# Kernel tuning notes

Measured on AMD Instinct MI355X. Metric: run time of the kernel, lower is better.

Reference implementation:

```python
import jax, jax.numpy as jnp
import numpy as np
from jax import lax

N, D = 65536, 6
NUM_SAMPLES, NUM_GROUPS, EMBED_DIM = 2048, 64, 512
EPS = 1e-5


def farthest_point_sampling(points_xyz, num_samples, key):
    # Sequential FPS via lax.scan: squared-euclidean min-distance update + argmax.
    n = points_xyz.shape[0]
    first = jax.random.randint(key, (), 0, n)
    dists0 = jnp.full((n,), jnp.inf, dtype=points_xyz.dtype)

    def step(carry, _):
        dists, last = carry
        d = jnp.sum((points_xyz - points_xyz[last]) ** 2, axis=-1)  # [n]
        dists = jnp.minimum(dists, d)
        dists = dists.at[last].set(-jnp.inf)  # never re-pick sampled points
        nxt = jnp.argmax(dists)
        return (dists, nxt), nxt

    (_, _), rest = lax.scan(step, (dists0, first), None, length=num_samples - 1)
    return jnp.concatenate([first[None], rest])  # [num_samples]


def bn(x, scale, bias):
    # flax nn.BatchNorm (training stats): normalize over all axes but the last.
    mean = x.mean(axis=(0, 1), keepdims=True)
    var = x.var(axis=(0, 1), keepdims=True)
    return scale * (x - mean) * lax.rsqrt(var + EPS) + bias


def setup_inputs() -> dict:
    key = jax.random.key(0)
    ks = jax.random.split(key, 3)
    points = jax.random.normal(ks[0], (N, D), dtype=jnp.float32)
    W1 = jax.random.normal(ks[1], (2 * D, EMBED_DIM), dtype=jnp.float32) * (1.0 / np.sqrt(2 * D))
    W2 = jax.random.normal(ks[2], (EMBED_DIM, EMBED_DIM), dtype=jnp.float32) * (1.0 / np.sqrt(EMBED_DIM))
    return {
        "points": points,
        "W1": W1, "b1": jnp.zeros((EMBED_DIM,), jnp.float32),
        "scale1": jnp.ones((EMBED_DIM,), jnp.float32), "bias1": jnp.zeros((EMBED_DIM,), jnp.float32),
        "W2": W2, "b2": jnp.zeros((EMBED_DIM,), jnp.float32),
        "scale2": jnp.ones((EMBED_DIM,), jnp.float32), "bias2": jnp.zeros((EMBED_DIM,), jnp.float32),
        "random_key": 1,
    }


def reference(points, W1, b1, scale1, bias1, W2, b2, scale2, bias2, random_key):
    key = jax.random.key(random_key)
    points_xyz = points[:, :3]

    # 1) farthest point sampling -> centroid indices [S]
    sampled_ids = farthest_point_sampling(points_xyz, NUM_SAMPLES, key)
    centroids = points_xyz[sampled_ids]  # [S, 3]

    # 2) KNN via squared-euclidean cdist + approx top-k (matches lax.approx_max_k in source)
    dist = (jnp.sum(centroids ** 2, -1)[:, None]
            + jnp.sum(points_xyz ** 2, -1)[None, :]
            - 2.0 * centroids @ points_xyz.T)  # [S, N]
    groups = lax.approx_max_k(-dist, NUM_GROUPS)[1]  # [S, k] int32

    # 3) gather-group: concat(delta-to-centroid, raw features) -> [S, k, 2D]
    cluster = points[groups]                      # [S, k, D]
    centroid_full = points[sampled_ids]           # [S, D]
    delta = cluster - centroid_full[:, None, :]
    features = jnp.concatenate([delta, cluster], axis=-1)  # [S, k, 2D]

    # 4) Dense + BN + ReLU, twice
    h = jax.nn.relu(bn(features @ W1 + b1, scale1, bias1))  # [S, k, E]
    h = jax.nn.relu(bn(h @ W2 + b2, scale2, bias2))         # [S, k, E]

    # 5) max-pool over the group axis
    return jnp.max(h, axis=1)  # [S, E]
```

## Files before the change

kernel.cpp:

```cpp
#include <hip/hip_runtime.h>
#include <stdint.h>

#define N_PTS 65536
#define DIMS 6
#define NSAMP 2048
#define NGRP 64
#define EMB 512
#define ROWS (NSAMP*NGRP)
#define EPS_BN 1e-5f

#define FIRST_MODE 0

typedef __attribute__((ext_vector_type(8))) short short8;
typedef __attribute__((ext_vector_type(4))) float float4v;

__device__ __forceinline__ unsigned short f2bf(float f) {
  unsigned u = __float_as_uint(f);
  u += 0x7FFFu + ((u >> 16) & 1u);
  return (unsigned short)(u >> 16);
}

__device__ __forceinline__ void tf2x32(unsigned k0, unsigned k1, unsigned &x0, unsigned &x1) {
  unsigned ks[3] = {k0, k1, k0 ^ k1 ^ 0x1BD11BDAu};
  const unsigned R[8] = {13,15,26,6,17,29,16,24};
  x0 += ks[0]; x1 += ks[1];
#pragma unroll
  for (int g = 0; g < 5; ++g) {
#pragma unroll
    for (int j = 0; j < 4; ++j) {
      unsigned r = R[(g & 1) * 4 + j];
      x0 += x1;
      x1 = (x1 << r) | (x1 >> (32 - r));
      x1 ^= x0;
    }
    x0 += ks[(g + 1) % 3];
    x1 += ks[(g + 2) % 3] + (unsigned)(g + 1);
  }
}

__device__ __forceinline__ int compute_first(unsigned seed) {
  unsigned k0 = 0u, k1 = seed;
  unsigned s0, s1;
#if (FIRST_MODE == 0) || (FIRST_MODE == 1)
  { unsigned a0 = 0u, a1 = 1u; tf2x32(k0, k1, a0, a1); s0 = a0; s1 = a1; }
#else
  { unsigned p0 = 0u, p1 = 2u; tf2x32(k0, k1, p0, p1);
    unsigned q0 = 1u, q1 = 3u; tf2x32(k0, k1, q0, q1);
    s0 = p1; s1 = q1; }
#endif
  unsigned b0 = 0u, b1v = 0u; tf2x32(s0, s1, b0, b1v);
#if (FIRST_MODE == 0) || (FIRST_MODE == 3)
  unsigned bits = b0 ^ b1v;
#else
  unsigned bits = b0;
#endif
  return (int)(bits & 0xFFFFu);
}

#define FPSB 16
#define MEGA_BLOCKS 256
#define FPS_PPT 4
#define GB_CAND 512
#define H1B_S 520
#define MEGA_LDS 90112
#define FAST_TRIES 64
#define WARMUP_ITS 4
#define SLOTS ((NSAMP-1)*FPSB)

#define DPPMAX(x, ctrl) do { \
  unsigned _m = (unsigned)__builtin_amdgcn_update_dpp(0, (int)(x), (ctrl), 0xf, 0xf, true); \
  (x) = (x) > _m ? (x) : _m; } while (0)

__device__ __forceinline__ void st_u64_l2(unsigned long long* p, unsigned long long v) {
  asm volatile("global_store_dwordx2 %0, %1, off sc0" :: "v"(p), "v"(v) : "memory");
}
__device__ __forceinline__ unsigned long long ld_u64_l2(const unsigned long long* p) {
  unsigned long long r;
  asm volatile("global_load_dwordx2 %0, %1, off sc0\n\ts_waitcnt vmcnt(0)"
               : "=&v"(r) : "v"(p) : "memory");
  return r;
}

__global__ __launch_bounds__(256) void k_init(const float* __restrict__ pts,
    const float* __restrict__ W2, const int* __restrict__ seed_arr,
    unsigned long long* __restrict__ slot, float* __restrict__ stats,
    float* __restrict__ st2, unsigned short* __restrict__ W2T,
    float4* __restrict__ xyzw, int* __restrict__ sampled) {
  int tid = blockIdx.x * 256 + threadIdx.x;
  if (tid < N_PTS) {
    float x = pts[tid*6], y = pts[tid*6+1], z = pts[tid*6+2];
    float p2 = __fadd_rn(__fadd_rn(__fmul_rn(x,x), __fmul_rn(y,y)), __fmul_rn(z,z));
    xyzw[tid] = make_float4(x, y, z, p2);
  }
#pragma unroll
  for (int i = 0; i < 4; ++i) {
    int e = tid + i*65536;
    int c = e >> 9, k = e & 511;
    W2T[e] = f2bf(W2[k*EMB + c]);
  }
  if (tid < 2*SLOTS) slot[tid] = 0ull;
  if (tid < 4*EMB) stats[tid] = 0.f;
  if (tid < 32*1024) st2[tid] = 0.f;
  if (tid >= 1 && tid < NSAMP) sampled[tid] = -1;
  if (tid == 0) sampled[0] = compute_first((unsigned)seed_arr[0]);
}

__global__ __launch_bounds__(1024) void k_mega(
    const float4* __restrict__ xyzw, const float* __restrict__ pts,
    const float* __restrict__ W1, const float* __restrict__ b1,
    unsigned long long* __restrict__ slot, int* __restrict__ sampled,
    int* __restrict__ groups, float* __restrict__ gsum, float* __restrict__ gss) {
  extern __shared__ __align__(16) char smraw[];
  const int t = threadIdx.x;
  unsigned long long* mirror = slot + SLOTS;
  if ((blockIdx.x & 15) == 0) {
    unsigned long long* blkmax = (unsigned long long*)smraw;
    volatile int* winLDS = (volatile int*)(smraw + 256);
    const int b = blockIdx.x >> 4;
    const int T = b*1024 + t;
    const int lane = t & 63, wid = t >> 6;
    float px[FPS_PPT], py[FPS_PPT], pz[FPS_PPT], pd[FPS_PPT];
    unsigned nidxu[FPS_PPT];
#pragma unroll
    for (int i = 0; i < FPS_PPT; ++i) {
      float4 p = xyzw[T + 16384*i];
      px[i] = p.x; py[i] = p.y; pz[i] = p.z; pd[i] = __builtin_inff();
      nidxu[i] = 0xFFFFFFFFu - (unsigned)(T + 16384*i);
    }
    if (t == 0) { winLDS[0] = -1; winLDS[1] = -1; blkmax[0] = 0ull; blkmax[1] = 0ull; }
    int last = sampled[0] & 0xFFFF;
    bool slowlink = false;
    if (wid == 0) __builtin_amdgcn_s_setprio(3);
    __syncthreads();
    for (int it = 0; it < NSAMP-1; ++it) {
      const int p = it & 1;
      float4 cc = xyzw[last];
      unsigned long long best = 1ull;
#pragma unroll
      for (int i = 0; i < FPS_PPT; ++i) {
        float dx = __fsub_rn(px[i], cc.x);
        float dy = __fsub_rn(py[i], cc.y);
        float dz = __fsub_rn(pz[i], cc.z);
        float d = __fadd_rn(__fadd_rn(__fmul_rn(dx,dx), __fmul_rn(dy,dy)), __fmul_rn(dz,dz));
        pd[i] = fminf(pd[i], d);
        unsigned long long pk = ((unsigned long long)__float_as_uint(pd[i]) << 32)
                              | (unsigned long long)nidxu[i];
        best = best > pk ? best : pk;
      }
      unsigned myd = (unsigned)(best >> 32);
      unsigned r = myd;
      DPPMAX(r, 0x111);
      DPPMAX(r, 0x112);
      DPPMAX(r, 0x114);
      DPPMAX(r, 0x118);
      DPPMAX(r, 0x142);
      DPPMAX(r, 0x143);
      unsigned bd = (unsigned)__builtin_amdgcn_readlane((int)r, 63);
      unsigned long long tie = __ballot(myd == bd);
      unsigned long long wbest;
      if (__popcll(tie) == 1) {
        int wl = (int)__builtin_ctzll(tie);
        unsigned lo = (unsigned)__builtin_amdgcn_readlane((int)(unsigned)best, wl);
        wbest = ((unsigned long long)bd << 32) | (unsigned long long)lo;
      } else {
        wbest = best;
#pragma unroll
        for (int off = 32; off >= 1; off >>= 1) {
          unsigned long long o = __shfl_xor(wbest, off, 64);
          wbest = wbest > o ? wbest : o;
        }
      }
      if (lane == 0) atomicMax(&blkmax[p], wbest);
      __syncthreads();
      if (wid == 0) {
        if (lane == 0) {
          winLDS[1-p] = -1;
          unsigned long long m = blkmax[p];
          blkmax[p] = 0ull;
          st_u64_l2(&mirror[it*FPSB + b], m);
          __hip_atomic_store(&slot[it*FPSB + b], m,
                             __ATOMIC_RELAXED, __HIP_MEMORY_SCOPE_AGENT);
        }
        unsigned long long v = 0ull;
        if (lane < FPSB) {
          unsigned long long* spm = &mirror[it*FPSB + lane];
          unsigned long long* sp  = &slot[it*FPSB + lane];
          if (it >= WARMUP_ITS && !slowlink) {
            int tries = 0;
            do { v = ld_u64_l2(spm); } while (v == 0ull && ++tries < FAST_TRIES);
            if (v == 0ull) slowlink = true;
          }
          if (v == 0ull) {
            do { v = __hip_atomic_load(sp, __ATOMIC_RELAXED, __HIP_MEMORY_SCOPE_AGENT); }
            while (v == 0ull);
          }
        }
        unsigned pd32 = (unsigned)(v >> 32);
        unsigned r2 = pd32;
        DPPMAX(r2, 0x111);
        DPPMAX(r2, 0x112);
        DPPMAX(r2, 0x114);
        DPPMAX(r2, 0x118);
        unsigned bd2 = (unsigned)__builtin_amdgcn_readlane((int)r2, 15);
        unsigned long long tie2 = __ballot((lane < FPSB) && (pd32 == bd2));
        if (__popcll(tie2) == 1) {
          int wl2 = (int)__builtin_ctzll(tie2);
          unsigned lo2 = (unsigned)__builtin_amdgcn_readlane((int)(unsigned)v, wl2);
          v = ((unsigned long long)bd2 << 32) | (unsigned long long)lo2;
        } else {
#pragma unroll
          for (int off = 8; off >= 1; off >>= 1) {
            unsigned long long o = __shfl_xor(v, off, 64);
            v = v > o ? v : o;
          }
          v = __shfl(v, 0, 64);
        }
        int win = (int)(0xFFFFFFFFu - (unsigned)(v & 0xFFFFFFFFull)) & 0xFFFF;
        if (lane == 0) {
          if (b == 0)
            __hip_atomic_store((unsigned*)&sampled[it+1], (unsigned)win,
                               __ATOMIC_RELAXED, __HIP_MEMORY_SCOPE_AGENT);
          winLDS[p] = win;
        }
        last = win;
      } else {
        __builtin_amdgcn_s_setprio(0);
        int w = winLDS[p];
        while (w == -1) { __builtin_amdgcn_s_sleep(1); w = winLDS[p]; }
        __builtin_amdgcn_s_setprio(1);
        last = w;
      }
    }
  } else {
    unsigned* hist  = (unsigned*)smraw;
    unsigned* scan  = (unsigned*)(smraw + 32768);
    unsigned* candK = (unsigned*)(smraw + 36864);
    int*      candI = (int*)(smraw + 38912);
    float*    feat  = (float*)(smraw + 40960);
    float*    cf    = (float*)(smraw + 44032);
    unsigned* ctl   = (unsigned*)(smraw + 44064);
    volatile int* binfo = (volatile int*)(smraw + 44080);
    const int wkr = blockIdx.x - 1 - (blockIdx.x >> 4);
    for (int s = wkr; s < NSAMP; s += MEGA_BLOCKS - FPSB) {
      if (t == 0) {
        unsigned v = __hip_atomic_load((const unsigned*)&sampled[s],
                        __ATOMIC_RELAXED, __HIP_MEMORY_SCOPE_AGENT);
        while (v == 0xFFFFFFFFu) {
          __builtin_amdgcn_s_sleep(64);
          v = __hip_atomic_load((const unsigned*)&sampled[s],
                  __ATOMIC_RELAXED, __HIP_MEMORY_SCOPE_AGENT);
        }
        binfo[2] = (int)(v & 0xFFFFu);
        ctl[0] = 0u; ctl[1] = 0u;
      }
      for (int k = t; k < 8192; k += 1024) hist[k] = 0u;
      __syncthreads();
      const int sid = binfo[2];
      float4 c4 = xyzw[sid];
      const float cx=c4.x, cy=c4.y, cz=c4.z, c2=c4.w;
      for (int i = 0; i < N_PTS/1024; ++i) {
        int j = i*1024 + t;
        float4 p = xyzw[j];
        float dot = __fadd_rn(__fadd_rn(__fmul_rn(cx,p.x),__fmul_rn(cy,p.y)),__fmul_rn(cz,p.z));
        float d = __fsub_rn(__fadd_rn(c2, p.w), __fmul_rn(2.0f, dot));
        unsigned kb = __float_as_uint(d);
        kb ^= ((unsigned)((int)kb >> 31)) | 0x80000000u;
        atomicAdd(&hist[kb >> 19], 1u);
      }
      __syncthreads();
      unsigned ch = 0u;
      for (int k = 0; k < 8; ++k) ch += hist[t*8 + k];
      scan[t] = ch;
      __syncthreads();
      for (int off = 1; off < 1024; off <<= 1) {
        unsigned vv = (t >= off) ? scan[t - off] : 0u;
        __syncthreads();
        scan[t] += vv;
        __syncthreads();
      }
      unsigned inc = scan[t], before = inc - ch;
      if (before < NGRP && inc >= NGRP) {
        unsigned c = before;
        for (int k = 0; k < 8; ++k) {
          unsigned nb = hist[t*8 + k];
          if (c + nb >= NGRP) { binfo[0] = t*8 + k; binfo[1] = (int)c; break; }
          c += nb;
        }
      }
      __syncthreads();
      const unsigned B = (unsigned)binfo[0];
      const int bef = binfo[1];
      for (int i = 0; i < N_PTS/1024; ++i) {
        int j = i*1024 + t;
        float4 p = xyzw[j];
        float dot = __fadd_rn(__fadd_rn(__fmul_rn(cx,p.x),__fmul_rn(cy,p.y)),__fmul_rn(cz,p.z));
        float d = __fsub_rn(__fadd_rn(c2, p.w), __fmul_rn(2.0f, dot));
        unsigned kb = __float_as_uint(d);
        kb ^= ((unsigned)((int)kb >> 31)) | 0x80000000u;
        unsigned bin = kb >> 19;
        if (bin < B) {
          unsigned pos = atomicAdd(&ctl[0], 1u);
          groups[s*NGRP + pos] = j;
        } else if (bin == B) {
          unsigned ci = atomicAdd(&ctl[1], 1u);
          if (ci < GB_CAND) { candK[ci] = kb; candI[ci] = j; }
        }
      }
      __syncthreads();
      int M = ctl[1] < GB_CAND ? (int)ctl[1] : GB_CAND;
      int need = NGRP - bef;
      for (int c = t; c < M; c += 1024) {
        unsigned mk = candK[c]; int mi = candI[c];
        int rank = 0;
        for (int q = 0; q < M; ++q) {
          unsigned qk = candK[q];
          rank += (qk < mk || (qk == mk && candI[q] < mi)) ? 1 : 0;
        }
        if (rank < need) {
          unsigned pos = atomicAdd(&ctl[0], 1u);
          groups[s*NGRP + pos] = candI[c];
        }
      }
      __syncthreads();
      if (t == 0) {
        while (ctl[0] < NGRP) { groups[s*NGRP + ctl[0]] = 0; ctl[0]++; }
      }
      __syncthreads();
      if (t < DIMS) cf[t] = pts[sid*6 + t];
      __syncthreads();
      if (t < NGRP) {
        int g = groups[s*NGRP + t];
#pragma unroll
        for (int k = 0; k < DIMS; ++k) {
          float v = pts[g*6 + k];
          feat[t*12 + k] = v - cf[k];
          feat[t*12 + 6 + k] = v;
        }
      }
      __syncthreads();
      if (t < EMB) {
        float w[12];
#pragma unroll
        for (int k = 0; k < 12; ++k) w[k] = W1[k*EMB + t];
        float b = b1[t];
        float sum = 0.f, ss = 0.f;
        for (int r = 0; r < NGRP; ++r) {
          float y = b;
#pragma unroll
          for (int k = 0; k < 12; ++k) y += feat[r*12+k] * w[k];
          sum += y; ss += y*y;
        }
        atomicAdd(&gsum[t], sum);
        atomicAdd(&gss[t], ss);
      }
      __syncthreads();
    }
  }
}

__global__ __launch_bounds__(EMB) void k_finalize(const float* __restrict__ gsum,
    const float* __restrict__ gss, const float* __restrict__ scale,
    const float* __restrict__ bias, float* __restrict__ ac) {
  int c = threadIdx.x;
  float inv = 1.f / (float)ROWS;
  float mean = gsum[c] * inv;
  float var = gss[c] * inv - mean*mean;
  var = var < 0.f ? 0.f : var;
  float a = scale[c] * rsqrtf(var + EPS_BN);
  ac[c] = a; ac[EMB + c] = bias[c] - mean * a;
}

__global__ __launch_bounds__(EMB) void k_finalize2(const float* __restrict__ st2,
    const float* __restrict__ scale, const float* __restrict__ bias,
    float* __restrict__ ac) {
  int c = threadIdx.x;
  float sum = 0.f, ss = 0.f;
  for (int i = 0; i < 32; ++i) {
    sum += st2[i*1024 + c];
    ss  += st2[i*1024 + 512 + c];
  }
  float inv = 1.f / (float)ROWS;
  float mean = sum * inv;
  float var = ss * inv - mean*mean;
  var = var < 0.f ? 0.f : var;
  float a = scale[c] * rsqrtf(var + EPS_BN);
  ac[c] = a; ac[EMB + c] = bias[c] - mean * a;
}

__global__ __launch_bounds__(512, 4) void k_mlp(const float* __restrict__ pts,
    const int* __restrict__ sampled, const int* __restrict__ groups,
    const float* __restrict__ W1, const float* __restrict__ b1,
    const float* __restrict__ ac1, const unsigned short* __restrict__ W2T,
    const float* __restrict__ b2, const float* __restrict__ scale2,
    float* __restrict__ st2, float* __restrict__ y2sel) {
  const int s = blockIdx.x, t = threadIdx.x;
  extern __shared__ __align__(16) char smc[];
  float* feat = (float*)smc;
  float* cf   = (float*)(smc + 3072);
  unsigned short* h1b = (unsigned short*)(smc + 3104);
  if (t < DIMS) cf[t] = pts[sampled[s]*6 + t];
  __syncthreads();
  if (t < NGRP) {
    int g = groups[s*NGRP + t];
#pragma unroll
    for (int k = 0; k < DIMS; ++k) {
      float v = pts[g*6 + k];
      feat[t*12+k]   = v - cf[k];
      feat[t*12+6+k] = v;
    }
  }
  __syncthreads();
  {
    float w[12];
#pragma unroll
    for (int k = 0; k < 12; ++k) w[k] = W1[k*EMB + t];
    float b = b1[t], a1 = ac1[t], c1 = ac1[EMB + t];
    for (int r = 0; r < NGRP; ++r) {
      float y = b;
#pragma unroll
      for (int k = 0; k < 12; ++k) y += feat[r*12+k] * w[k];
      float hv = a1*y + c1;
      h1b[r*H1B_S + t] = f2bf(hv > 0.f ? hv : 0.f);
    }
  }
  __syncthreads();
  const int lane = t & 63, w = t >> 6;
  const int quad = lane >> 4, l16 = lane & 15;
  float4v acc[4][4];
#pragma unroll
  for (int nt = 0; nt < 4; ++nt) {
    float bv = b2[(w*4+nt)*16 + l16];
#pragma unroll
    for (int mt = 0; mt < 4; ++mt)
      acc[nt][mt] = (float4v){bv, bv, bv, bv};
  }
  for (int kc = 0; kc < 16; ++kc) {
    const int kb = kc*32 + quad*8;
    short8 af[4];
#pragma unroll
    for (int mt = 0; mt < 4; ++mt)
      af[mt] = *(const short8*)&h1b[(mt*16 + l16)*H1B_S + kb];
#pragma unroll
    for (int nt = 0; nt < 4; ++nt) {
      const int c = (w*4+nt)*16 + l16;
      short8 bf = *(const short8*)&W2T[c*EMB + kb];
#pragma unroll
      for (int mt = 0; mt < 4; ++mt)
        acc[nt][mt] = __builtin_amdgcn_mfma_f32_16x16x32_bf16(af[mt], bf, acc[nt][mt], 0, 0, 0);
    }
  }
#pragma unroll
  for (int nt = 0; nt < 4; ++nt) {
    float sm_ = 0.f, ss_ = 0.f, mx = -__builtin_inff(), mn = __builtin_inff();
#pragma unroll
    for (int mt = 0; mt < 4; ++mt)
#pragma unroll
      for (int i = 0; i < 4; ++i) {
        float v = acc[nt][mt][i];
        sm_ += v; ss_ += v*v;
        mx = fmaxf(mx, v); mn = fminf(mn, v);
      }
#pragma unroll
    for (int off = 16; off <= 32; off <<= 1) {
      sm_ += __shfl_xor(sm_, off, 64);
      ss_ += __shfl_xor(ss_, off, 64);
      mx = fmaxf(mx, __shfl_xor(mx, off, 64));
      mn = fminf(mn, __shfl_xor(mn, off, 64));
    }
    if (quad == 0) {
      int c = (w*4+nt)*16 + l16;
      atomicAdd(&st2[(s & 31)*1024 + c], sm_);
      atomicAdd(&st2[(s & 31)*1024 + 512 + c], ss_);
      y2sel[s*EMB + c] = (scale2[c] >= 0.f) ? mx : mn;
    }
  }
}

__global__ __launch_bounds__(256) void k_out(const float* __restrict__ y2sel,
    const float* __restrict__ ac2, float* __restrict__ out) {
  int i = blockIdx.x*256 + threadIdx.x;
  int c = i & (EMB-1);
  float a = ac2[c], cc = ac2[EMB + c];
  float v = a*y2sel[i] + cc;
  out[i] = v > 0.f ? v : 0.f;
}

extern "C" void kernel_launch(void* const* d_in, const int* in_sizes, int n_in,
                              void* d_out, int out_size, void* d_ws, size_t ws_size,
                              hipStream_t stream) {
  const float* pts    = (const float*)d_in[0];
  const float* W1     = (const float*)d_in[1];
  const float* b1     = (const float*)d_in[2];
  const float* scale1 = (const float*)d_in[3];
  const float* bias1  = (const float*)d_in[4];
  const float* W2     = (const float*)d_in[5];
  const float* b2     = (const float*)d_in[6];
  const float* scale2 = (const float*)d_in[7];
  const float* bias2  = (const float*)d_in[8];
  const int*   seed   = (const int*)d_in[9];
  float* out = (float*)d_out;

  char* ws = (char*)d_ws;
  int*    sampled = (int*)(ws);
  int*    groups  = (int*)(ws + 8192);
  float4* xyzw    = (float4*)(ws + 532480);
  float*  stats   = (float*)(ws + 1581056);
  float* gsum1 = stats, *gss1 = stats + 512;
  float*  ac1     = (float*)(ws + 1589248);
  float*  ac2     = (float*)(ws + 1593344);
  float*  y2sel   = (float*)(ws + 1597440);
  unsigned long long* slot = (unsigned long long*)(ws + 1597440);
  unsigned short* W2T = (unsigned short*)(ws + 5791744);
  float* st2      = (float*)(ws + 6316032);

  k_init<<<256, 256, 0, stream>>>(pts, W2, seed, slot, stats, st2, W2T, xyzw, sampled);
  k_mega<<<MEGA_BLOCKS, 1024, MEGA_LDS, stream>>>(xyzw, pts, W1, b1, slot, sampled,
                                                  groups, gsum1, gss1);
  k_finalize<<<1, EMB, 0, stream>>>(gsum1, gss1, scale1, bias1, ac1);
  size_t mlp_lds = 3104 + (size_t)NGRP * H1B_S * sizeof(unsigned short);
  k_mlp<<<NSAMP, 512, mlp_lds, stream>>>(pts, sampled, groups, W1, b1, ac1,
                                         W2T, b2, scale2, st2, y2sel);
  k_finalize2<<<1, EMB, 0, stream>>>(st2, scale2, bias2, ac2);
  k_out<<<(out_size+255)/256, 256, 0, stream>>>(y2sel, ac2, out);
}
```

Before: 3.872 ms.

## Replace per-block atomicMax and syncthreads in FPS with per-wave tagged ring slots

In the farthest-point-sampling loop, each wavefront now publishes its tagged best candidate straight into a global double-buffered ring of 256 slots. The block-level LDS atomicMax and __syncthreads are removed. The lead wave of every FPS block polls all 256 slots with vectorized dwordx4 L2 loads and uses iteration tags to tell fresh entries from stale ones, then does a full-wave reduction to pick the winner. This takes a block barrier and an LDS atomic off the serial 2047-step critical path. In exchange the lead wave does more global reads per iteration and relies on tag-based staleness checks, with indices packed into 16 bits.

```diff
diff --git a/kernel.cpp b/kernel.cpp
--- a/kernel.cpp
+++ b/kernel.cpp
@@ -13,6 +13,7 @@
 
 typedef __attribute__((ext_vector_type(8))) short short8;
 typedef __attribute__((ext_vector_type(4))) float float4v;
+typedef __attribute__((ext_vector_type(4))) unsigned uint4v;
 
 __device__ __forceinline__ unsigned short f2bf(float f) {
   unsigned u = __float_as_uint(f);
@@ -65,7 +66,7 @@
 #define MEGA_LDS 90112
 #define FAST_TRIES 64
 #define WARMUP_ITS 4
-#define SLOTS ((NSAMP-1)*FPSB)
+#define RING_W 256
 
 #define DPPMAX(x, ctrl) do { \
   unsigned _m = (unsigned)__builtin_amdgcn_update_dpp(0, (int)(x), (ctrl), 0xf, 0xf, true); \
@@ -74,11 +75,12 @@
 __device__ __forceinline__ void st_u64_l2(unsigned long long* p, unsigned long long v) {
   asm volatile("global_store_dwordx2 %0, %1, off sc0" :: "v"(p), "v"(v) : "memory");
 }
-__device__ __forceinline__ unsigned long long ld_u64_l2(const unsigned long long* p) {
-  unsigned long long r;
-  asm volatile("global_load_dwordx2 %0, %1, off sc0\n\ts_waitcnt vmcnt(0)"
-               : "=&v"(r) : "v"(p) : "memory");
-  return r;
+__device__ __forceinline__ void ld_slots_l2(const unsigned long long* p,
+                                            uint4v &a, uint4v &c) {
+  asm volatile("global_load_dwordx4 %0, %2, off sc0\n\t"
+               "global_load_dwordx4 %1, %2, off offset:16 sc0\n\t"
+               "s_waitcnt vmcnt(0)"
+               : "=&v"(a), "=&v"(c) : "v"(p) : "memory");
 }
 
 __global__ __launch_bounds__(256) void k_init(const float* __restrict__ pts,
@@ -98,7 +100,7 @@
     int c = e >> 9, k = e & 511;
     W2T[e] = f2bf(W2[k*EMB + c]);
   }
-  if (tid < 2*SLOTS) slot[tid] = 0ull;
+  if (tid < 4*RING_W) slot[tid] = 0ull;
   if (tid < 4*EMB) stats[tid] = 0.f;
   if (tid < 32*1024) st2[tid] = 0.f;
   if (tid >= 1 && tid < NSAMP) sampled[tid] = -1;
@@ -112,13 +114,15 @@
     int* __restrict__ groups, float* __restrict__ gsum, float* __restrict__ gss) {
   extern __shared__ __align__(16) char smraw[];
   const int t = threadIdx.x;
-  unsigned long long* mirror = slot + SLOTS;
   if ((blockIdx.x & 15) == 0) {
-    unsigned long long* blkmax = (unsigned long long*)smraw;
-    volatile int* winLDS = (volatile int*)(smraw + 256);
+    volatile int* winLDS = (volatile int*)smraw;
+    unsigned long long* mirR = slot;
+    unsigned long long* canR = slot + 2*RING_W;
     const int b = blockIdx.x >> 4;
     const int T = b*1024 + t;
     const int lane = t & 63, wid = t >> 6;
+    const int gw = b*16 + wid;
+    const bool isLead = (wid == 0);
     float px[FPS_PPT], py[FPS_PPT], pz[FPS_PPT], pd[FPS_PPT];
     unsigned nidxu[FPS_PPT];
 #pragma unroll
@@ -127,13 +131,13 @@
       px[i] = p.x; py[i] = p.y; pz[i] = p.z; pd[i] = __builtin_inff();
       nidxu[i] = 0xFFFFFFFFu - (unsigned)(T + 16384*i);
     }
-    if (t == 0) { winLDS[0] = -1; winLDS[1] = -1; blkmax[0] = 0ull; blkmax[1] = 0ull; }
+    if (t == 0) winLDS[0] = 0;
     int last = sampled[0] & 0xFFFF;
-    bool slowlink = false;
-    if (wid == 0) __builtin_amdgcn_s_setprio(3);
+    bool slow = false;
+    if (isLead) __builtin_amdgcn_s_setprio(3);
     __syncthreads();
     for (int it = 0; it < NSAMP-1; ++it) {
-      const int p = it & 1;
+      const unsigned tag = (unsigned)(it + 1);
       float4 cc = xyzw[last];
       unsigned long long best = 1ull;
 #pragma unroll
@@ -170,65 +174,92 @@
           wbest = wbest > o ? wbest : o;
         }
       }
-      if (lane == 0) atomicMax(&blkmax[p], wbest);
-      __syncthreads();
-      if (wid == 0) {
-        if (lane == 0) {
-          winLDS[1-p] = -1;
-          unsigned long long m = blkmax[p];
-          blkmax[p] = 0ull;
-          st_u64_l2(&mirror[it*FPSB + b], m);
-          __hip_atomic_store(&slot[it*FPSB + b], m,
-                             __ATOMIC_RELAXED, __HIP_MEMORY_SCOPE_AGENT);
-        }
-        unsigned long long v = 0ull;
-        if (lane < FPSB) {
-          unsigned long long* spm = &mirror[it*FPSB + lane];
-          unsigned long long* sp  = &slot[it*FPSB + lane];
-          if (it >= WARMUP_ITS && !slowlink) {
-            int tries = 0;
-            do { v = ld_u64_l2(spm); } while (v == 0ull && ++tries < FAST_TRIES);
-            if (v == 0ull) slowlink = true;
+      unsigned widx = 0xFFFFFFFFu - (unsigned)wbest;
+      unsigned long long sv = ((wbest >> 32) << 32)
+                            | ((unsigned long long)(tag & 0xFFFFu) << 16)
+                            | (unsigned long long)(0xFFFFu - (widx & 0xFFFFu));
+      if (lane == 0) {
+        st_u64_l2(&mirR[(it & 1)*RING_W + gw], sv);
+        __hip_atomic_store(&canR[(it & 1)*RING_W + gw], sv,
+                           __ATOMIC_RELAXED, __HIP_MEMORY_SCOPE_AGENT);
+      }
+      if (isLead) {
+        const int pg = (it & 1)*RING_W + lane*4;
+        const unsigned tagw = tag & 0xFFFFu;
+        const unsigned staleT = (it >= 2) ? (unsigned)((it - 1) & 0xFFFF) : 0u;
+        unsigned long long v0, v1, v2, v3;
+        bool useFast = (!slow) && (it >= WARMUP_ITS);
+        int tries = 0;
+        for (;;) {
+          if (useFast) {
+            uint4v a, c;
+            ld_slots_l2(&mirR[pg], a, c);
+            v0 = ((unsigned long long)a[1] << 32) | a[0];
+            v1 = ((unsigned long long)a[3] << 32) | a[2];
+            v2 = ((unsigned long long)c[1] << 32) | c[0];
+            v3 = ((unsigned long long)c[3] << 32) | c[2];
+          } else {
+            v0 = __hip_atomic_load(&canR[pg+0], __ATOMIC_RELAXED, __HIP_MEMORY_SCOPE_AGENT);
+            v1 = __hip_atomic_load(&canR[pg+1], __ATOMIC_RELAXED, __HIP_MEMORY_SCOPE_AGENT);
+            v2 = __hip_atomic_load(&canR[pg+2], __ATOMIC_RELAXED, __HIP_MEMORY_SCOPE_AGENT);
+            v3 = __hip_atomic_load(&canR[pg+3], __ATOMIC_RELAXED, __HIP_MEMORY_SCOPE_AGENT);
           }
-          if (v == 0ull) {
-            do { v = __hip_atomic_load(sp, __ATOMIC_RELAXED, __HIP_MEMORY_SCOPE_AGENT); }
-            while (v == 0ull);
+          unsigned t0 = ((unsigned)v0 >> 16) & 0xFFFFu;
+          unsigned t1 = ((unsigned)v1 >> 16) & 0xFFFFu;
+          unsigned t2 = ((unsigned)v2 >> 16) & 0xFFFFu;
+          unsigned t3 = ((unsigned)v3 >> 16) & 0xFFFFu;
+          bool anystale = (t0 == staleT) || (t1 == staleT) ||
+                          (t2 == staleT) || (t3 == staleT);
+          if (__ballot(anystale) == 0ull) {
+            if (t0 != tagw) v0 = 0ull;
+            if (t1 != tagw) v1 = 0ull;
+            if (t2 != tagw) v2 = 0ull;
+            if (t3 != tagw) v3 = 0ull;
+            break;
           }
-        }
-        unsigned pd32 = (unsigned)(v >> 32);
-        unsigned r2 = pd32;
+          if (useFast && ++tries >= FAST_TRIES) { slow = true; useFast = false; }
+        }
+        unsigned long long m01 = v0 > v1 ? v0 : v1;
+        unsigned long long m23 = v2 > v3 ? v2 : v3;
+        unsigned long long lm  = m01 > m23 ? m01 : m23;
+        unsigned ld_ = (unsigned)(lm >> 32);
+        unsigned r2 = ld_;
         DPPMAX(r2, 0x111);
         DPPMAX(r2, 0x112);
         DPPMAX(r2, 0x114);
         DPPMAX(r2, 0x118);
-        unsigned bd2 = (unsigned)__builtin_amdgcn_readlane((int)r2, 15);
-        unsigned long long tie2 = __ballot((lane < FPSB) && (pd32 == bd2));
+        DPPMAX(r2, 0x142);
+        DPPMAX(r2, 0x143);
+        unsigned bd2 = (unsigned)__builtin_amdgcn_readlane((int)r2, 63);
+        unsigned long long tie2 = __ballot(ld_ == bd2);
+        unsigned long long gbest;
         if (__popcll(tie2) == 1) {
           int wl2 = (int)__builtin_ctzll(tie2);
-          unsigned lo2 = (unsigned)__builtin_amdgcn_readlane((int)(unsigned)v, wl2);
-          v = ((unsigned long long)bd2 << 32) | (unsigned long long)lo2;
+          unsigned lo2 = (unsigned)__builtin_amdgcn_readlane((int)(unsigned)lm, wl2);
+          gbest = ((unsigned long long)bd2 << 32) | (unsigned long long)lo2;
         } else {
-#pragma unroll
-          for (int off = 8; off >= 1; off >>= 1) {
-            unsigned long long o = __shfl_xor(v, off, 64);
-            v = v > o ? v : o;
+          gbest = lm;
+#pragma unroll
+          for (int off = 32; off >= 1; off >>= 1) {
+            unsigned long long o = __shfl_xor(gbest, off, 64);
+            gbest = gbest > o ? gbest : o;
           }
-          v = __shfl(v, 0, 64);
-        }
-        int win = (int)(0xFFFFFFFFu - (unsigned)(v & 0xFFFFFFFFull)) & 0xFFFF;
+          gbest = __shfl(gbest, 0, 64);
+        }
+        int win = (int)(0xFFFFu - ((unsigned)gbest & 0xFFFFu));
         if (lane == 0) {
           if (b == 0)
             __hip_atomic_store((unsigned*)&sampled[it+1], (unsigned)win,
                                __ATOMIC_RELAXED, __HIP_MEMORY_SCOPE_AGENT);
-          winLDS[p] = win;
+          winLDS[0] = (int)((tag << 16) | (unsigned)win);
         }
         last = win;
       } else {
         __builtin_amdgcn_s_setprio(0);
-        int w = winLDS[p];
-        while (w == -1) { __builtin_amdgcn_s_sleep(1); w = winLDS[p]; }
+        int w = winLDS[0];
+        while (((unsigned)w >> 16) != tag) { __builtin_amdgcn_s_sleep(1); w = winLDS[0]; }
         __builtin_amdgcn_s_setprio(1);
-        last = w;
+        last = w & 0xFFFF;
       }
     }
   } else {
@@ -398,7 +429,7 @@
   float* feat = (float*)smc;
   float* cf   = (float*)(smc + 3072);
   unsigned short* h1b = (unsigned short*)(smc + 3104);
-  if (t < DIMS) cf[t] = pts[sampled[s]*6 + t];
+  if (t < DIMS) cf[t] = pts[(sampled[s] & 0xFFFF)*6 + t];
   __syncthreads();
   if (t < NGRP) {
     int g = groups[s*NGRP + t];
```

Measured after the change: 10.32 ms. +166.6%, slower.
